# Performance work log

Hardware: AMD Instinct MI355X
Metric: run time of the kernel (lower is better)

## Reference

```python
import jax, jax.numpy as jnp
import numpy as np

N_KNOTS = 16384
BATCH = 256
N_SAMP = 32768


def setup_inputs() -> dict:
    key = jax.random.key(0)
    k1, k2, k3 = jax.random.split(key, 3)
    # strictly increasing knot abscissae (matches module assumption of sorted x_points)
    incs = jax.random.uniform(k1, (N_KNOTS,), minval=0.01, maxval=1.0, dtype=jnp.float32)
    x_points = jnp.cumsum(incs)
    y_points = jax.random.normal(k2, (N_KNOTS,), dtype=jnp.float32)
    # samples must have a valid right bracket: x in [x_points[0], x_points[N-2])
    lo = x_points[0]
    hi = x_points[N_KNOTS - 2]
    u = jax.random.uniform(k3, (BATCH, N_SAMP), dtype=jnp.float32)
    x_samp = lo + u * (hi - lo) * 0.999
    return {"x_samp": x_samp, "x_points": x_points, "y_points": y_points}


def reference(x_samp, x_points, y_points):
    # Original: masked argmin over (x_samp - x_points) with negatives set to inf,
    # i.e. index of the largest knot <= x_samp. Equivalent to searchsorted(right)-1.
    idxi = jnp.searchsorted(x_points, x_samp, side='right') - 1  # [B, S]
    idxf = idxi + 1
    xi = x_points[idxi]  # [B, S] gather
    xf = x_points[idxf]
    yi = y_points[idxi]
    yf = y_points[idxf]
    ds = (x_samp - xi) / (xf - xi)
    return yi + ds * (yf - yi)
```

## Files before the change

kernel.cpp:

```cpp
#include <hip/hip_runtime.h>


#define NB 14336
#define NKMAX 16384

typedef float f32x4 __attribute__((ext_vector_type(4)));

__device__ __forceinline__ int bucket_of(float v, float lo, float inv_w) {
    return (int)((v - lo) * inv_w);
}

__device__ __forceinline__ unsigned pack_ys(float y, float s) {
    _Float16 hy = (_Float16)y, hs = (_Float16)s;
    unsigned short uy = __builtin_bit_cast(unsigned short, hy);
    unsigned short us = __builtin_bit_cast(unsigned short, hs);
    return (unsigned)uy | ((unsigned)us << 16);
}

__global__ void build_tbl(const float* __restrict__ xp, const float* __restrict__ yp,
                          unsigned* __restrict__ ysg, unsigned short* __restrict__ tbl,
                          int nk) {
    int i = blockIdx.x * blockDim.x + threadIdx.x;
    float lo = xp[0];
    float inv_w = (float)NB / (xp[nk - 1] - lo);
    if (i < nk) {
        float y0 = yp[i];
        float slope = 0.0f;
        if (i < nk - 1) slope = (yp[i + 1] - y0) / (xp[i + 1] - xp[i]);
        ysg[i] = pack_ys(y0, slope);
    }
    if (i < NB) {
        int loj = -1, hij = nk - 1;
        while (loj < hij) {
            int mid = (loj + hij + 1) >> 1;
            if (bucket_of(xp[mid], lo, inv_w) <= i) loj = mid; else hij = mid - 1;
        }
        int v = loj;
        if (v < 0) v = 0;
        if (v > nk - 2) v = nk - 2;
        tbl[i] = (unsigned short)v;
    }
}

__global__ __launch_bounds__(1024) void interp(
        const f32x4* __restrict__ xs4, const float* __restrict__ xp,
        const unsigned* __restrict__ ysg, const unsigned short* __restrict__ tbl,
        f32x4* __restrict__ out4, int n4, int nk) {
    __shared__ float sx[NKMAX];
    __shared__ unsigned sys[NKMAX];
    __shared__ unsigned short sT[NB];

    for (int i = threadIdx.x; i < nk; i += 1024) {
        sx[i] = xp[i];
        sys[i] = ysg[i];
    }
    for (int i = threadIdx.x; i < NB; i += 1024)
        sT[i] = tbl[i];

    float lo = xp[0];
    float inv_w = (float)NB / (xp[nk - 1] - lo);
    __syncthreads();

    int stride = gridDim.x * blockDim.x;
    for (int t = blockIdx.x * blockDim.x + threadIdx.x; t < n4; t += stride) {
        f32x4 xv = __builtin_nontemporal_load(&xs4[t]);
        float x[4] = {xv.x, xv.y, xv.z, xv.w};
        int loi[4], hii[4];
        #pragma unroll
        for (int k = 0; k < 4; k++) {
            int b = bucket_of(x[k], lo, inv_w);
            b = min(max(b, 0), NB - 1);
            hii[k] = sT[b];
            loi[k] = b ? (int)sT[b - 1] : 0;
        }
        bool again = (hii[0] > loi[0]) | (hii[1] > loi[1]) |
                     (hii[2] > loi[2]) | (hii[3] > loi[3]);
        while (again) {
            #pragma unroll
            for (int k = 0; k < 4; k++) {
                if (hii[k] > loi[k]) {
                    int mid = (loi[k] + hii[k] + 1) >> 1;
                    if (sx[mid] <= x[k]) loi[k] = mid; else hii[k] = mid - 1;
                }
            }
            again = (hii[0] > loi[0]) | (hii[1] > loi[1]) |
                    (hii[2] > loi[2]) | (hii[3] > loi[3]);
        }
        f32x4 r;
        #pragma unroll
        for (int k = 0; k < 4; k++) {
            unsigned u = sys[loi[k]];
            float hy = (float)__builtin_bit_cast(_Float16, (unsigned short)(u & 0xffffu));
            float hs = (float)__builtin_bit_cast(_Float16, (unsigned short)(u >> 16));
            r[k] = fmaf(x[k] - sx[loi[k]], hs, hy);
        }
        __builtin_nontemporal_store(r, &out4[t]);
    }
}

extern "C" void kernel_launch(void* const* d_in, const int* in_sizes, int n_in,
                              void* d_out, int out_size, void* d_ws, size_t ws_size,
                              hipStream_t stream) {
    const float* xs = (const float*)d_in[0];
    const float* xp = (const float*)d_in[1];
    const float* yp = (const float*)d_in[2];
    int ns = in_sizes[0];
    int nk = in_sizes[1];

    unsigned* ysg = (unsigned*)d_ws;
    unsigned short* tbl = (unsigned short*)((char*)d_ws + (size_t)nk * sizeof(unsigned));

    int na = (nk > NB ? nk : NB);
    build_tbl<<<(na + 255) / 256, 256, 0, stream>>>(xp, yp, ysg, tbl, nk);

    int n4 = ns / 4;
    interp<<<256, 1024, 0, stream>>>((const f32x4*)xs, xp, ysg, tbl,
                                     (f32x4*)d_out, n4, nk);
}
```

Measured before the change: 107.4 us.

## Pack bucket bounds, process eight samples per thread with branchless search steps

The bucket table now stores both the lower and upper knot bounds in one 32-bit entry, which halves the number of table lookups, and the bucket count is reduced. Each thread handles two float4 vectors (eight samples) at once for more ILP, runs three unrolled branchless bisection steps, and then finishes with a per-sample loop. The shared-memory preloads are vectorized. Fewer buckets mean wider intervals and possibly more LDS reads per sample.

```diff
diff --git a/kernel.cpp b/kernel.cpp
--- a/kernel.cpp
+++ b/kernel.cpp
@@ -1,7 +1,7 @@
 #include <hip/hip_runtime.h>
 
 
-#define NB 14336
+#define NB 7936
 #define NKMAX 16384
 
 typedef float f32x4 __attribute__((ext_vector_type(4)));
@@ -17,8 +17,20 @@
     return (unsigned)uy | ((unsigned)us << 16);
 }
 
+__device__ __forceinline__ int hi_of_bucket(const float* xp, int nk, float lo,
+                                            float inv_w, int b) {
+    int loj = -1, hij = nk - 1;
+    while (loj < hij) {
+        int mid = (loj + hij + 1) >> 1;
+        if (bucket_of(xp[mid], lo, inv_w) <= b) loj = mid; else hij = mid - 1;
+    }
+    if (loj < 0) loj = 0;
+    if (loj > nk - 2) loj = nk - 2;
+    return loj;
+}
+
 __global__ void build_tbl(const float* __restrict__ xp, const float* __restrict__ yp,
-                          unsigned* __restrict__ ysg, unsigned short* __restrict__ tbl,
+                          unsigned* __restrict__ ysg, unsigned* __restrict__ tbl,
                           int nk) {
     int i = blockIdx.x * blockDim.x + threadIdx.x;
     float lo = xp[0];
@@ -30,71 +42,77 @@
         ysg[i] = pack_ys(y0, slope);
     }
     if (i < NB) {
-        int loj = -1, hij = nk - 1;
-        while (loj < hij) {
-            int mid = (loj + hij + 1) >> 1;
-            if (bucket_of(xp[mid], lo, inv_w) <= i) loj = mid; else hij = mid - 1;
-        }
-        int v = loj;
-        if (v < 0) v = 0;
-        if (v > nk - 2) v = nk - 2;
-        tbl[i] = (unsigned short)v;
+        int hi = hi_of_bucket(xp, nk, lo, inv_w, i);
+        int lo16 = (i > 0) ? hi_of_bucket(xp, nk, lo, inv_w, i - 1) : 0;
+        tbl[i] = (unsigned)lo16 | ((unsigned)hi << 16);
     }
 }
 
 __global__ __launch_bounds__(1024) void interp(
         const f32x4* __restrict__ xs4, const float* __restrict__ xp,
-        const unsigned* __restrict__ ysg, const unsigned short* __restrict__ tbl,
+        const unsigned* __restrict__ ysg, const unsigned* __restrict__ tbl,
         f32x4* __restrict__ out4, int n4, int nk) {
     __shared__ float sx[NKMAX];
     __shared__ unsigned sys[NKMAX];
-    __shared__ unsigned short sT[NB];
+    __shared__ unsigned sT[NB];
 
-    for (int i = threadIdx.x; i < nk; i += 1024) {
-        sx[i] = xp[i];
-        sys[i] = ysg[i];
-    }
-    for (int i = threadIdx.x; i < NB; i += 1024)
-        sT[i] = tbl[i];
+    const f32x4* xp4 = (const f32x4*)xp;
+    f32x4* sx4 = (f32x4*)sx;
+    for (int i = threadIdx.x; i < nk / 4; i += 1024) sx4[i] = xp4[i];
+    const uint4* ysg4 = (const uint4*)ysg;
+    uint4* sys4 = (uint4*)sys;
+    for (int i = threadIdx.x; i < nk / 4; i += 1024) sys4[i] = ysg4[i];
+    for (int i = threadIdx.x; i < NB; i += 1024) sT[i] = tbl[i];
 
     float lo = xp[0];
     float inv_w = (float)NB / (xp[nk - 1] - lo);
     __syncthreads();
 
-    int stride = gridDim.x * blockDim.x;
-    for (int t = blockIdx.x * blockDim.x + threadIdx.x; t < n4; t += stride) {
-        f32x4 xv = __builtin_nontemporal_load(&xs4[t]);
-        float x[4] = {xv.x, xv.y, xv.z, xv.w};
-        int loi[4], hii[4];
+    int tid = blockIdx.x * blockDim.x + threadIdx.x;
+    int T = gridDim.x * blockDim.x;
+    for (int t = tid; t < n4; t += 2 * T) {
+        int t2 = t + T;
+        bool has2 = (t2 < n4);
+        f32x4 xa = __builtin_nontemporal_load(&xs4[t]);
+        f32x4 xb = has2 ? __builtin_nontemporal_load(&xs4[t2]) : xa;
+        float x[8] = {xa.x, xa.y, xa.z, xa.w, xb.x, xb.y, xb.z, xb.w};
+        int loi[8], hii[8];
         #pragma unroll
-        for (int k = 0; k < 4; k++) {
+        for (int k = 0; k < 8; k++) {
             int b = bucket_of(x[k], lo, inv_w);
             b = min(max(b, 0), NB - 1);
-            hii[k] = sT[b];
-            loi[k] = b ? (int)sT[b - 1] : 0;
+            unsigned p = sT[b];
+            loi[k] = (int)(p & 0xffffu);
+            hii[k] = (int)(p >> 16);
         }
-        bool again = (hii[0] > loi[0]) | (hii[1] > loi[1]) |
-                     (hii[2] > loi[2]) | (hii[3] > loi[3]);
-        while (again) {
+        #pragma unroll
+        for (int r = 0; r < 3; r++) {
             #pragma unroll
-            for (int k = 0; k < 4; k++) {
-                if (hii[k] > loi[k]) {
-                    int mid = (loi[k] + hii[k] + 1) >> 1;
-                    if (sx[mid] <= x[k]) loi[k] = mid; else hii[k] = mid - 1;
-                }
+            for (int k = 0; k < 8; k++) {
+                int mid = (loi[k] + hii[k] + 1) >> 1;
+                bool ge = (sx[mid] <= x[k]);
+                loi[k] = ge ? mid : loi[k];
+                hii[k] = ge ? hii[k] : mid - 1;
             }
-            again = (hii[0] > loi[0]) | (hii[1] > loi[1]) |
-                    (hii[2] > loi[2]) | (hii[3] > loi[3]);
         }
-        f32x4 r;
         #pragma unroll
-        for (int k = 0; k < 4; k++) {
+        for (int k = 0; k < 8; k++) {
+            while (hii[k] > loi[k]) {
+                int mid = (loi[k] + hii[k] + 1) >> 1;
+                if (sx[mid] <= x[k]) loi[k] = mid; else hii[k] = mid - 1;
+            }
+        }
+        f32x4 ra, rb;
+        #pragma unroll
+        for (int k = 0; k < 8; k++) {
             unsigned u = sys[loi[k]];
             float hy = (float)__builtin_bit_cast(_Float16, (unsigned short)(u & 0xffffu));
             float hs = (float)__builtin_bit_cast(_Float16, (unsigned short)(u >> 16));
-            r[k] = fmaf(x[k] - sx[loi[k]], hs, hy);
+            float v = fmaf(x[k] - sx[loi[k]], hs, hy);
+            if (k < 4) ra[k] = v; else rb[k - 4] = v;
         }
-        __builtin_nontemporal_store(r, &out4[t]);
+        __builtin_nontemporal_store(ra, &out4[t]);
+        if (has2) __builtin_nontemporal_store(rb, &out4[t2]);
     }
 }
 
@@ -108,7 +126,7 @@
     int nk = in_sizes[1];
 
     unsigned* ysg = (unsigned*)d_ws;
-    unsigned short* tbl = (unsigned short*)((char*)d_ws + (size_t)nk * sizeof(unsigned));
+    unsigned* tbl = (unsigned*)((char*)d_ws + (size_t)nk * sizeof(unsigned));
 
     int na = (nk > NB ? nk : NB);
     build_tbl<<<(na + 255) / 256, 256, 0, stream>>>(xp, yp, ysg, tbl, nk);
```

Result: faster. 103.9 us (-3.3%).

## Replace bucketed binary search with aligned 8-wide vector window scan

Applied to the files above, without the earlier changes.

The per-bucket table now stores the start knot of each bucket, and the interpolation kernel replaces the divergent binary-search loop with two 128-bit LDS reads of x and packed y/slope around the aligned start. It then does a branchless select across 8 candidates, with a rare linear-scan fallback. The global-to-LDS preload is vectorized and padded with +inf sentinels. Input loads are software-pipelined by prefetching the next two float4 chunks, and each thread processes two chunks per iteration. This trades wave divergence and dependent LDS round trips for more registers and wider LDS accesses. It relies on nk being a multiple of 4 and buckets rarely spanning more than 8 knots.

```diff
diff --git a/kernel.cpp b/kernel.cpp
--- a/kernel.cpp
+++ b/kernel.cpp
@@ -3,8 +3,10 @@
 
 #define NB 14336
 #define NKMAX 16384
+#define PAD 16
 
-typedef float f32x4 __attribute__((ext_vector_type(4)));
+typedef float    f32x4 __attribute__((ext_vector_type(4)));
+typedef unsigned u32x4 __attribute__((ext_vector_type(4)));
 
 __device__ __forceinline__ int bucket_of(float v, float lo, float inv_w) {
     return (int)((v - lo) * inv_w);
@@ -15,6 +17,12 @@
     unsigned short uy = __builtin_bit_cast(unsigned short, hy);
     unsigned short us = __builtin_bit_cast(unsigned short, hs);
     return (unsigned)uy | ((unsigned)us << 16);
+}
+
+__device__ __forceinline__ float lerp_ys(float dx, unsigned u) {
+    float hy = (float)__builtin_bit_cast(_Float16, (unsigned short)(u & 0xffffu));
+    float hs = (float)__builtin_bit_cast(_Float16, (unsigned short)(u >> 16));
+    return fmaf(dx, hs, hy);
 }
 
 __global__ void build_tbl(const float* __restrict__ xp, const float* __restrict__ yp,
@@ -30,14 +38,15 @@
         ysg[i] = pack_ys(y0, slope);
     }
     if (i < NB) {
-        int loj = -1, hij = nk - 1;
-        while (loj < hij) {
-            int mid = (loj + hij + 1) >> 1;
-            if (bucket_of(xp[mid], lo, inv_w) <= i) loj = mid; else hij = mid - 1;
+        int v = 0;
+        if (i > 0) {
+            int loj = -1, hij = nk - 1;
+            while (loj < hij) {
+                int mid = (loj + hij + 1) >> 1;
+                if (bucket_of(xp[mid], lo, inv_w) <= i - 1) loj = mid; else hij = mid - 1;
+            }
+            v = loj < 0 ? 0 : (loj > nk - 2 ? nk - 2 : loj);
         }
-        int v = loj;
-        if (v < 0) v = 0;
-        if (v > nk - 2) v = nk - 2;
         tbl[i] = (unsigned short)v;
     }
 }
@@ -46,55 +55,90 @@
         const f32x4* __restrict__ xs4, const float* __restrict__ xp,
         const unsigned* __restrict__ ysg, const unsigned short* __restrict__ tbl,
         f32x4* __restrict__ out4, int n4, int nk) {
-    __shared__ float sx[NKMAX];
-    __shared__ unsigned sys[NKMAX];
+    __shared__ __align__(16) float sx[NKMAX + PAD];
+    __shared__ __align__(16) unsigned sys[NKMAX + PAD];
     __shared__ unsigned short sT[NB];
 
-    for (int i = threadIdx.x; i < nk; i += 1024) {
-        sx[i] = xp[i];
-        sys[i] = ysg[i];
+    {
+        const f32x4* xp4 = (const f32x4*)xp;
+        f32x4* sx4w = (f32x4*)sx;
+        for (int i = threadIdx.x; i < nk / 4; i += 1024) sx4w[i] = xp4[i];
+        const u32x4* ysg4 = (const u32x4*)ysg;
+        u32x4* sys4w = (u32x4*)sys;
+        for (int i = threadIdx.x; i < nk / 4; i += 1024) sys4w[i] = ysg4[i];
+        for (int i = threadIdx.x; i < NB; i += 1024) sT[i] = tbl[i];
+        if (threadIdx.x < PAD) {
+            sx[nk + threadIdx.x] = __builtin_inff();
+            sys[nk + threadIdx.x] = 0u;
+        }
     }
-    for (int i = threadIdx.x; i < NB; i += 1024)
-        sT[i] = tbl[i];
 
     float lo = xp[0];
     float inv_w = (float)NB / (xp[nk - 1] - lo);
     __syncthreads();
 
-    int stride = gridDim.x * blockDim.x;
-    for (int t = blockIdx.x * blockDim.x + threadIdx.x; t < n4; t += stride) {
-        f32x4 xv = __builtin_nontemporal_load(&xs4[t]);
-        float x[4] = {xv.x, xv.y, xv.z, xv.w};
-        int loi[4], hii[4];
+    const f32x4* sx4 = (const f32x4*)sx;
+    const u32x4* sys4 = (const u32x4*)sys;
+
+    int tid = blockIdx.x * blockDim.x + threadIdx.x;
+    int T = gridDim.x * blockDim.x;
+
+    int t = tid;
+    f32x4 xa, xb;
+    bool has1 = (t < n4), has2 = (t + T < n4);
+    if (has1) xa = __builtin_nontemporal_load(&xs4[t]);
+    if (has2) xb = __builtin_nontemporal_load(&xs4[t + T]);
+
+    while (has1) {
+        int tn = t + 2 * T;
+        f32x4 xan, xbn;
+        bool h1n = (tn < n4), h2n = (tn + T < n4);
+        if (h1n) xan = __builtin_nontemporal_load(&xs4[tn]);
+        if (h2n) xbn = __builtin_nontemporal_load(&xs4[tn + T]);
+
+        f32x4 res[2];
         #pragma unroll
-        for (int k = 0; k < 4; k++) {
-            int b = bucket_of(x[k], lo, inv_w);
-            b = min(max(b, 0), NB - 1);
-            hii[k] = sT[b];
-            loi[k] = b ? (int)sT[b - 1] : 0;
-        }
-        bool again = (hii[0] > loi[0]) | (hii[1] > loi[1]) |
-                     (hii[2] > loi[2]) | (hii[3] > loi[3]);
-        while (again) {
+        for (int half = 0; half < 2; half++) {
+            f32x4 xq = (half == 0) ? xa : xb;
+            float x[4] = {xq.x, xq.y, xq.z, xq.w};
+            int al[4];
+            f32x4 wx0[4], wx1[4];
+            u32x4 wy0[4], wy1[4];
             #pragma unroll
             for (int k = 0; k < 4; k++) {
-                if (hii[k] > loi[k]) {
-                    int mid = (loi[k] + hii[k] + 1) >> 1;
-                    if (sx[mid] <= x[k]) loi[k] = mid; else hii[k] = mid - 1;
+                int b = bucket_of(x[k], lo, inv_w);
+                b = min(max(b, 0), NB - 1);
+                al[k] = ((int)sT[b]) & ~3;
+                int q = al[k] >> 2;
+                wx0[k] = sx4[q];
+                wx1[k] = sx4[q + 1];
+                wy0[k] = sys4[q];
+                wy1[k] = sys4[q + 1];
+            }
+            #pragma unroll
+            for (int k = 0; k < 4; k++) {
+                float xk = x[k];
+                float xi = wx0[k].x; unsigned ys = wy0[k].x;
+                if (wx0[k].y <= xk) { xi = wx0[k].y; ys = wy0[k].y; }
+                if (wx0[k].z <= xk) { xi = wx0[k].z; ys = wy0[k].z; }
+                if (wx0[k].w <= xk) { xi = wx0[k].w; ys = wy0[k].w; }
+                if (wx1[k].x <= xk) { xi = wx1[k].x; ys = wy1[k].x; }
+                if (wx1[k].y <= xk) { xi = wx1[k].y; ys = wy1[k].y; }
+                if (wx1[k].z <= xk) { xi = wx1[k].z; ys = wy1[k].z; }
+                bool tail = (wx1[k].w <= xk);
+                if (tail) { xi = wx1[k].w; ys = wy1[k].w; }
+                if (tail) {
+                    int j = al[k] + 7;
+                    while (sx[j + 1] <= xk) j++;
+                    xi = sx[j]; ys = sys[j];
                 }
+                res[half][k] = lerp_ys(xk - xi, ys);
             }
-            again = (hii[0] > loi[0]) | (hii[1] > loi[1]) |
-                    (hii[2] > loi[2]) | (hii[3] > loi[3]);
         }
-        f32x4 r;
-        #pragma unroll
-        for (int k = 0; k < 4; k++) {
-            unsigned u = sys[loi[k]];
-            float hy = (float)__builtin_bit_cast(_Float16, (unsigned short)(u & 0xffffu));
-            float hs = (float)__builtin_bit_cast(_Float16, (unsigned short)(u >> 16));
-            r[k] = fmaf(x[k] - sx[loi[k]], hs, hy);
-        }
-        __builtin_nontemporal_store(r, &out4[t]);
+        __builtin_nontemporal_store(res[0], &out4[t]);
+        if (has2) __builtin_nontemporal_store(res[1], &out4[t + T]);
+
+        t = tn; xa = xan; xb = xbn; has1 = h1n; has2 = h2n;
     }
 }
 
```

Result: no change. 106.9 us (-0.5%).
